# Optimization experiments

Measured on AMD Instinct MI355X. Metric: run time of the kernel, lower is better.

The kernel has to match this reference:

```python
import jax, jax.numpy as jnp
import numpy as np

D_MODEL = 1024
NUM_HEADS = 16
HEAD_DIM = D_MODEL // NUM_HEADS
B, S = 4, 2048


def setup_inputs() -> dict:
    key = jax.random.key(0)
    ks = jax.random.split(key, 11)
    scale = 1.0 / np.sqrt(D_MODEL)
    return {
        "query": jax.random.normal(ks[0], (B, S, D_MODEL), dtype=jnp.float32),
        "key": jax.random.normal(ks[1], (B, S, D_MODEL), dtype=jnp.float32),
        "value": jax.random.normal(ks[2], (B, S, D_MODEL), dtype=jnp.float32),
        "Wq": jax.random.normal(ks[3], (D_MODEL, D_MODEL), dtype=jnp.float32) * scale,
        "bq": jnp.zeros((D_MODEL,), dtype=jnp.float32),
        "Wk": jax.random.normal(ks[4], (D_MODEL, D_MODEL), dtype=jnp.float32) * scale,
        "bk": jnp.zeros((D_MODEL,), dtype=jnp.float32),
        "Wv": jax.random.normal(ks[5], (D_MODEL, D_MODEL), dtype=jnp.float32) * scale,
        "bv": jnp.zeros((D_MODEL,), dtype=jnp.float32),
        "Wo": jax.random.normal(ks[6], (D_MODEL, D_MODEL), dtype=jnp.float32) * scale,
        "bo": jnp.zeros((D_MODEL,), dtype=jnp.float32),
    }


def reference(query, key, value, Wq, bq, Wk, bk, Wv, bv, Wo, bo):
    b = query.shape[0]
    # QKV projections, split into heads: [B, H, S, hd]
    Q = (query @ Wq + bq).reshape(b, -1, NUM_HEADS, HEAD_DIM).transpose(0, 2, 1, 3)
    K = (key @ Wk + bk).reshape(b, -1, NUM_HEADS, HEAD_DIM).transpose(0, 2, 1, 3)
    V = (value @ Wv + bv).reshape(b, -1, NUM_HEADS, HEAD_DIM).transpose(0, 2, 1, 3)
    # scaled dot-product attention, full [B, H, S, S] scores (as in original)
    scores = jnp.einsum("bhqd,bhkd->bhqk", Q, K) / jnp.sqrt(
        jnp.asarray(HEAD_DIM, dtype=jnp.float32))
    attn = jax.nn.softmax(scores, axis=-1)
    out = jnp.einsum("bhqk,bhkd->bhqd", attn, V)
    out = out.transpose(0, 2, 1, 3).reshape(b, -1, D_MODEL)
    return out @ Wo + bo
```

## Files before the change

### kernel.cpp

```cpp
#include <hip/hip_runtime.h>
#include <hip/hip_bf16.h>

typedef _Float16 f16;
typedef _Float16 f16x8 __attribute__((ext_vector_type(8)));
typedef _Float16 f16x4 __attribute__((ext_vector_type(4)));
typedef __fp16 h16x2 __attribute__((ext_vector_type(2)));
typedef float f32x4 __attribute__((ext_vector_type(4)));

#define D_MODEL 1024
#define NHEAD 16
#define HD 64
#define BATCH 4
#define SEQ 2048
#define TOK (BATCH * SEQ)

__device__ __forceinline__ void gload_lds16(const void* g, void* l) {
  __builtin_amdgcn_global_load_lds(
      (const __attribute__((address_space(1))) unsigned int*)g,
      (__attribute__((address_space(3))) unsigned int*)l, 16, 0, 0);
}

__device__ __forceinline__ f16x8 fragF16_64(const char* rowptr, int g, int c) {
  union { uint4 u; f16x8 v; } r;
  r.u = *reinterpret_cast<const uint4*>(rowptr + ((g * 16) ^ ((c & 3) << 4)));
  return r.v;
}
__device__ __forceinline__ f16x8 fragF32_128(const char* rowptr, int g, int c) {
  const int s = (c & 7) << 4;
  union { uint4 u; float f[4]; } a, b;
  a.u = *reinterpret_cast<const uint4*>(rowptr + ((g * 32) ^ s));
  b.u = *reinterpret_cast<const uint4*>(rowptr + ((g * 32 + 16) ^ s));
  f16x8 r;
  r[0] = (f16)a.f[0]; r[1] = (f16)a.f[1]; r[2] = (f16)a.f[2]; r[3] = (f16)a.f[3];
  r[4] = (f16)b.f[0]; r[5] = (f16)b.f[1]; r[6] = (f16)b.f[2]; r[7] = (f16)b.f[3];
  return r;
}
__device__ __forceinline__ f16x8 lds_frag(const char* rowptr, int cb0, int s) {
  const uint2 a = *reinterpret_cast<const uint2*>(rowptr + (cb0 ^ s));
  const uint2 b = *reinterpret_cast<const uint2*>(rowptr + ((cb0 + 32) ^ s));
  union { unsigned int u[4]; f16x8 v; } r;
  r.u[0] = a.x; r.u[1] = a.y; r.u[2] = b.x; r.u[3] = b.y;
  return r.v;
}

__global__ __launch_bounds__(256) void transpose_cvt4_k(
    const float* __restrict__ w0, const float* __restrict__ w1,
    const float* __restrict__ w2, const float* __restrict__ w3,
    f16* __restrict__ t0, f16* __restrict__ t1, f16* __restrict__ t2,
    f16* __restrict__ t3) {
  __shared__ float tile[32][33];
  const float* W = blockIdx.z == 0 ? w0 : blockIdx.z == 1 ? w1 : blockIdx.z == 2 ? w2 : w3;
  f16* Wt = blockIdx.z == 0 ? t0 : blockIdx.z == 1 ? t1 : blockIdx.z == 2 ? t2 : t3;
  int n0 = blockIdx.x * 32, k0 = blockIdx.y * 32;
  int tx = threadIdx.x & 31, ty = threadIdx.x >> 5;
#pragma unroll
  for (int i = 0; i < 32; i += 8)
    tile[ty + i][tx] = W[(size_t)(k0 + ty + i) * D_MODEL + n0 + tx];
  __syncthreads();
#pragma unroll
  for (int i = 0; i < 32; i += 8)
    Wt[(size_t)(n0 + ty + i) * D_MODEL + k0 + tx] = (f16)tile[tx][ty + i];
}

template <bool A_F32, bool B_F32, bool OUT_F32, bool BIAS_ROW>
__global__ __launch_bounds__(256) void gemm_k(
    const void* __restrict__ Ap, const void* __restrict__ Bp,
    const float* __restrict__ bias, void* __restrict__ Cout,
    int M, int N, int K, float scale) {
  constexpr int ABUF = A_F32 ? 16384 : 8192;
  constexpr int BBUF = B_F32 ? 16384 : 8192;
  constexpr int BUF = ABUF + BBUF;
  constexpr int NA = A_F32 ? 4 : 2;
  constexpr int NB = B_F32 ? 4 : 2;
  __shared__ char smem[2 * BUF];
  const int tid = threadIdx.x;
  const int lane = tid & 63, wid = tid >> 6;
  const int g = lane >> 4, c = lane & 15;
  const int wm = wid >> 1, wn = wid & 1;
  const size_t brow = (size_t)blockIdx.y * 128, bcol = (size_t)blockIdx.x * 128;

  f32x4 acc[4][4];
#pragma unroll
  for (int i = 0; i < 4; ++i)
#pragma unroll
    for (int j = 0; j < 4; ++j) acc[i][j] = (f32x4){0.f, 0.f, 0.f, 0.f};

  const char* ga[NA];
  const char* gb[NB];
#pragma unroll
  for (int j = 0; j < NA; ++j) {
    int ch = wid * NA + j;
    if constexpr (A_F32) {
      int row = ch * 8 + (lane >> 3);
      ga[j] = (const char*)Ap + ((size_t)(brow + row) * K) * 4 +
              (((lane & 7) * 16) ^ ((row & 7) << 4));
    } else {
      int row = ch * 16 + (lane >> 2);
      ga[j] = (const char*)Ap + ((size_t)(brow + row) * K) * 2 +
              (((lane & 3) * 16) ^ ((row & 3) << 4));
    }
  }
#pragma unroll
  for (int j = 0; j < NB; ++j) {
    int ch = wid * NB + j;
    if constexpr (B_F32) {
      int row = ch * 8 + (lane >> 3);
      gb[j] = (const char*)Bp + ((size_t)(bcol + row) * K) * 4 +
              (((lane & 7) * 16) ^ ((row & 7) << 4));
    } else {
      int row = ch * 16 + (lane >> 2);
      gb[j] = (const char*)Bp + ((size_t)(bcol + row) * K) * 2 +
              (((lane & 3) * 16) ^ ((row & 3) << 4));
    }
  }
  auto stage = [&](char* buf) {
#pragma unroll
    for (int j = 0; j < NA; ++j) {
      gload_lds16(ga[j], buf + (wid * NA + j) * 1024);
      ga[j] += A_F32 ? 128 : 64;
    }
#pragma unroll
    for (int j = 0; j < NB; ++j) {
      gload_lds16(gb[j], buf + ABUF + (wid * NB + j) * 1024);
      gb[j] += B_F32 ? 128 : 64;
    }
  };

  stage(smem);
  const int nt = K / 32;
  for (int t = 0; t < nt; ++t) {
    char* cur = smem + (size_t)(t & 1) * BUF;
    char* nxt = smem + (size_t)((t + 1) & 1) * BUF;
    asm volatile("s_waitcnt vmcnt(0)" ::: "memory");
    __syncthreads();
    if (t + 1 < nt) stage(nxt);

    f16x8 Af[4], Bf[4];
#pragma unroll
    for (int fm = 0; fm < 4; ++fm) {
      int row = wm * 64 + fm * 16 + c;
      if constexpr (A_F32) Af[fm] = fragF32_128(cur + row * 128, g, c);
      else Af[fm] = fragF16_64(cur + row * 64, g, c);
    }
#pragma unroll
    for (int fn = 0; fn < 4; ++fn) {
      int row = wn * 64 + fn * 16 + c;
      if constexpr (B_F32) Bf[fn] = fragF32_128(cur + ABUF + row * 128, g, c);
      else Bf[fn] = fragF16_64(cur + ABUF + row * 64, g, c);
    }
#pragma unroll
    for (int fm = 0; fm < 4; ++fm)
#pragma unroll
      for (int fn = 0; fn < 4; ++fn)
        acc[fm][fn] = __builtin_amdgcn_mfma_f32_16x16x32_f16(Af[fm], Bf[fn],
                                                             acc[fm][fn], 0, 0, 0);
  }

#pragma unroll
  for (int fn = 0; fn < 4; ++fn) {
    size_t col = bcol + wn * 64 + fn * 16 + c;
    float cbias = BIAS_ROW ? 0.f : bias[col];
#pragma unroll
    for (int fm = 0; fm < 4; ++fm) {
#pragma unroll
      for (int r = 0; r < 4; ++r) {
        size_t row = brow + wm * 64 + fm * 16 + g * 4 + r;
        float v = (acc[fm][fn][r] + (BIAS_ROW ? bias[row] : cbias)) * scale;
        if (OUT_F32)
          ((float*)Cout)[row * (size_t)N + col] = v;
        else
          ((f16*)Cout)[row * (size_t)N + col] = (f16)v;
      }
    }
  }
}

__global__ __launch_bounds__(512) void attn_k(const f16* __restrict__ Q,
                                              const f16* __restrict__ Kp,
                                              const f16* __restrict__ Vt,
                                              f16* __restrict__ AO) {
  __shared__ char smem[32768];
  const int tid = threadIdx.x, lane = tid & 63, wid = tid >> 6;
  const int g = lane >> 4, c = lane & 15;
  const int b = blockIdx.x >> 4, h = blockIdx.x & 15;
  const int qt = blockIdx.y;
  const size_t qrow0 = (size_t)b * SEQ + (size_t)qt * 256;
  const int sr = lane >> 3;
  const int sc = (lane & 7) * 16;
  const float NEG_M = -8.65617025f;

#pragma unroll
  for (int j = 0; j < 4; ++j) {
    int ch = wid * 4 + j;
    int row = ch * 8 + sr;
    const char* gq = (const char*)Q + ((qrow0 + row) * D_MODEL + h * HD) * 2 +
                     (sc ^ (sr << 4));
    gload_lds16(gq, smem + ch * 1024);
  }
  asm volatile("s_waitcnt vmcnt(0)" ::: "memory");
  __syncthreads();

  f16x8 Qf[2][2];
#pragma unroll
  for (int fq = 0; fq < 2; ++fq) {
    int row = wid * 32 + fq * 16 + c;
#pragma unroll
    for (int kk = 0; kk < 2; ++kk) {
      union { uint4 u; f16x8 v; } r;
      r.u = *reinterpret_cast<const uint4*>(
          smem + row * 128 + ((kk * 64 + g * 16) ^ ((c & 7) << 4)));
      Qf[fq][kk] = r.v;
    }
  }
  __syncthreads();

  const char* gk;
  const char* gv;
  {
    int row = wid * 8 + sr;
    gk = (const char*)Kp + (((size_t)b * SEQ + row) * D_MODEL + h * HD) * 2 +
         (sc ^ (sr << 4));
    gv = (const char*)Vt + ((size_t)(h * HD + row) * TOK + (size_t)b * SEQ) * 2 +
         (sc ^ (sr << 4));
  }
  gload_lds16(gk, smem + wid * 1024);
  gload_lds16(gv, smem + 8192 + wid * 1024);
  gk += (size_t)64 * D_MODEL * 2;
  gv += 64 * 2;

  f16x8 ones_f;
#pragma unroll
  for (int j = 0; j < 8; ++j) ones_f[j] = (c == 0) ? (f16)1.0f : (f16)0.0f;

  f32x4 o[4][2];
#pragma unroll
  for (int i = 0; i < 4; ++i)
#pragma unroll
    for (int j = 0; j < 2; ++j) o[i][j] = (f32x4){0.f, 0.f, 0.f, 0.f};
  f32x4 o_l[2] = {(f32x4){0.f, 0.f, 0.f, 0.f}, (f32x4){0.f, 0.f, 0.f, 0.f}};

  for (int t = 0; t < SEQ / 64; ++t) {
    char* cur = smem + (size_t)(t & 1) * 16384;
    char* nxt = smem + (size_t)((t + 1) & 1) * 16384;
    asm volatile("s_waitcnt vmcnt(0)" ::: "memory");
    __syncthreads();
    if (t + 1 < SEQ / 64) {
      gload_lds16(gk, nxt + wid * 1024);
      gload_lds16(gv, nxt + 8192 + wid * 1024);
      gk += (size_t)64 * D_MODEL * 2;
      gv += 64 * 2;
    }
    const char* Ks = cur;
    const char* Vs = cur + 8192;

    f32x4 st[4][2];
#pragma unroll
    for (int i = 0; i < 4; ++i)
#pragma unroll
      for (int j = 0; j < 2; ++j)
        st[i][j] = (f32x4){NEG_M, NEG_M, NEG_M, NEG_M};
#pragma unroll
    for (int kk = 0; kk < 2; ++kk) {
      f16x8 Kf[4];
#pragma unroll
      for (int km = 0; km < 4; ++km) {
        int row = km * 16 + c;
        union { uint4 u; f16x8 v; } r;
        r.u = *reinterpret_cast<const uint4*>(
            Ks + row * 128 + ((kk * 64 + g * 16) ^ ((c & 7) << 4)));
        Kf[km] = r.v;
      }
      __builtin_amdgcn_s_setprio(1);
#pragma unroll
      for (int km = 0; km < 4; ++km)
#pragma unroll
        for (int fq = 0; fq < 2; ++fq)
          st[km][fq] = __builtin_amdgcn_mfma_f32_16x16x32_f16(Kf[km], Qf[fq][kk],
                                                              st[km][fq], 0, 0, 0);
      __builtin_amdgcn_s_setprio(0);
    }

    f16x8 pb[2][2];
#pragma unroll
    for (int fq = 0; fq < 2; ++fq) {
#pragma unroll
      for (int km = 0; km < 4; ++km)
#pragma unroll
        for (int r = 0; r < 4; ++r)
          st[km][fq][r] = __builtin_amdgcn_exp2f(st[km][fq][r]);
#pragma unroll
      for (int k2 = 0; k2 < 2; ++k2) {
        union { h16x2 h2[4]; f16x8 v; } u;
        u.h2[0] = __builtin_amdgcn_cvt_pkrtz(st[2 * k2][fq][0], st[2 * k2][fq][1]);
        u.h2[1] = __builtin_amdgcn_cvt_pkrtz(st[2 * k2][fq][2], st[2 * k2][fq][3]);
        u.h2[2] = __builtin_amdgcn_cvt_pkrtz(st[2 * k2 + 1][fq][0], st[2 * k2 + 1][fq][1]);
        u.h2[3] = __builtin_amdgcn_cvt_pkrtz(st[2 * k2 + 1][fq][2], st[2 * k2 + 1][fq][3]);
        pb[k2][fq] = u.v;
      }
    }

#pragma unroll
    for (int k2 = 0; k2 < 2; ++k2) {
      f16x8 Vf[4];
#pragma unroll
      for (int fhd = 0; fhd < 4; ++fhd) {
        int row = fhd * 16 + c;
        Vf[fhd] = lds_frag(Vs + row * 128, k2 * 64 + g * 8, (row & 7) << 4);
      }
      __builtin_amdgcn_s_setprio(1);
#pragma unroll
      for (int fhd = 0; fhd < 4; ++fhd)
#pragma unroll
        for (int fq = 0; fq < 2; ++fq)
          o[fhd][fq] = __builtin_amdgcn_mfma_f32_16x16x32_f16(Vf[fhd], pb[k2][fq],
                                                              o[fhd][fq], 0, 0, 0);
#pragma unroll
      for (int fq = 0; fq < 2; ++fq)
        o_l[fq] = __builtin_amdgcn_mfma_f32_16x16x32_f16(ones_f, pb[k2][fq],
                                                         o_l[fq], 0, 0, 0);
      __builtin_amdgcn_s_setprio(0);
    }
  }

#pragma unroll
  for (int fq = 0; fq < 2; ++fq) {
    float L = __shfl(o_l[fq][0], c);
    float rl = 1.0f / L;
    size_t token = qrow0 + wid * 32 + fq * 16 + c;
#pragma unroll
    for (int fhd = 0; fhd < 4; ++fhd) {
      f16x4 vv;
#pragma unroll
      for (int r = 0; r < 4; ++r) vv[r] = (f16)(o[fhd][fq][r] * rl);
      *reinterpret_cast<f16x4*>(AO + token * D_MODEL + h * HD + fhd * 16 + g * 4) = vv;
    }
  }
}

extern "C" void kernel_launch(void* const* d_in, const int* in_sizes, int n_in,
                              void* d_out, int out_size, void* d_ws, size_t ws_size,
                              hipStream_t stream) {
  const float* q32 = (const float*)d_in[0];
  const float* k32 = (const float*)d_in[1];
  const float* v32 = (const float*)d_in[2];
  const float* Wq = (const float*)d_in[3];
  const float* bq = (const float*)d_in[4];
  const float* Wk = (const float*)d_in[5];
  const float* bk = (const float*)d_in[6];
  const float* Wv = (const float*)d_in[7];
  const float* bv = (const float*)d_in[8];
  const float* Wo = (const float*)d_in[9];
  const float* bo = (const float*)d_in[10];

  const size_t TOKD = (size_t)TOK * D_MODEL;
  const size_t WD = (size_t)D_MODEL * D_MODEL;
  f16* Qp = (f16*)d_ws;
  f16* Kp = Qp + TOKD;
  f16* Vt = Kp + TOKD;
  f16* AO = Vt + TOKD;
  f16* Wqt = AO + TOKD;
  f16* Wkt = Wqt + WD;
  f16* Wvt = Wkt + WD;
  f16* Wot = Wvt + WD;

  dim3 tg(32, 32, 4);
  transpose_cvt4_k<<<tg, 256, 0, stream>>>(Wq, Wk, Wv, Wo, Wqt, Wkt, Wvt, Wot);

  dim3 gq(D_MODEL / 128, TOK / 128);
  gemm_k<true, false, false, false><<<gq, 256, 0, stream>>>(
      q32, Wqt, bq, Qp, TOK, D_MODEL, D_MODEL, 0.18033688f);
  gemm_k<true, false, false, false><<<gq, 256, 0, stream>>>(
      k32, Wkt, bk, Kp, TOK, D_MODEL, D_MODEL, 1.0f);
  dim3 gv(TOK / 128, D_MODEL / 128);
  gemm_k<false, true, false, true><<<gv, 256, 0, stream>>>(
      Wvt, v32, bv, Vt, D_MODEL, TOK, D_MODEL, 1.0f);

  dim3 ga(BATCH * NHEAD, SEQ / 256);
  attn_k<<<ga, 512, 0, stream>>>(Qp, Kp, Vt, AO);

  gemm_k<false, false, true, false><<<gq, 256, 0, stream>>>(
      AO, Wot, bo, (float*)d_out, TOK, D_MODEL, D_MODEL, 1.0f);
}
```

Before: 228.1 us.

## Deepen attention K/V prefetch to four stages and use 8-wave GEMM blocks

The attention kernel's K/V staging goes from double buffering to a 4-slot ring with three tiles in flight. Partial vmcnt waits let it consume the oldest tile while newer loads are still pending, which is meant to hide global-load latency; LDS use doubles to 64 KB per block. Separately, the GEMM kernel moves from 256 to 512 threads per 128x128 tile, with each wave computing a 32x64 sub-tile instead of 64x64. This gives more waves for latency hiding but halves MFMA work per fragment load.

```diff
diff --git a/kernel.cpp b/kernel.cpp
--- a/kernel.cpp
+++ b/kernel.cpp
@@ -63,15 +63,15 @@
 }
 
 template <bool A_F32, bool B_F32, bool OUT_F32, bool BIAS_ROW>
-__global__ __launch_bounds__(256) void gemm_k(
+__global__ __launch_bounds__(512) void gemm_k(
     const void* __restrict__ Ap, const void* __restrict__ Bp,
     const float* __restrict__ bias, void* __restrict__ Cout,
     int M, int N, int K, float scale) {
   constexpr int ABUF = A_F32 ? 16384 : 8192;
   constexpr int BBUF = B_F32 ? 16384 : 8192;
   constexpr int BUF = ABUF + BBUF;
-  constexpr int NA = A_F32 ? 4 : 2;
-  constexpr int NB = B_F32 ? 4 : 2;
+  constexpr int NA = A_F32 ? 2 : 1;
+  constexpr int NB = B_F32 ? 2 : 1;
   __shared__ char smem[2 * BUF];
   const int tid = threadIdx.x;
   const int lane = tid & 63, wid = tid >> 6;
@@ -79,9 +79,9 @@
   const int wm = wid >> 1, wn = wid & 1;
   const size_t brow = (size_t)blockIdx.y * 128, bcol = (size_t)blockIdx.x * 128;
 
-  f32x4 acc[4][4];
-#pragma unroll
-  for (int i = 0; i < 4; ++i)
+  f32x4 acc[2][4];
+#pragma unroll
+  for (int i = 0; i < 2; ++i)
 #pragma unroll
     for (int j = 0; j < 4; ++j) acc[i][j] = (f32x4){0.f, 0.f, 0.f, 0.f};
 
@@ -135,10 +135,10 @@
     __syncthreads();
     if (t + 1 < nt) stage(nxt);
 
-    f16x8 Af[4], Bf[4];
-#pragma unroll
-    for (int fm = 0; fm < 4; ++fm) {
-      int row = wm * 64 + fm * 16 + c;
+    f16x8 Af[2], Bf[4];
+#pragma unroll
+    for (int fm = 0; fm < 2; ++fm) {
+      int row = wm * 32 + fm * 16 + c;
       if constexpr (A_F32) Af[fm] = fragF32_128(cur + row * 128, g, c);
       else Af[fm] = fragF16_64(cur + row * 64, g, c);
     }
@@ -149,7 +149,7 @@
       else Bf[fn] = fragF16_64(cur + ABUF + row * 64, g, c);
     }
 #pragma unroll
-    for (int fm = 0; fm < 4; ++fm)
+    for (int fm = 0; fm < 2; ++fm)
 #pragma unroll
       for (int fn = 0; fn < 4; ++fn)
         acc[fm][fn] = __builtin_amdgcn_mfma_f32_16x16x32_f16(Af[fm], Bf[fn],
@@ -161,10 +161,10 @@
     size_t col = bcol + wn * 64 + fn * 16 + c;
     float cbias = BIAS_ROW ? 0.f : bias[col];
 #pragma unroll
-    for (int fm = 0; fm < 4; ++fm) {
+    for (int fm = 0; fm < 2; ++fm) {
 #pragma unroll
       for (int r = 0; r < 4; ++r) {
-        size_t row = brow + wm * 64 + fm * 16 + g * 4 + r;
+        size_t row = brow + wm * 32 + fm * 16 + g * 4 + r;
         float v = (acc[fm][fn][r] + (BIAS_ROW ? bias[row] : cbias)) * scale;
         if (OUT_F32)
           ((float*)Cout)[row * (size_t)N + col] = v;
@@ -179,7 +179,7 @@
                                               const f16* __restrict__ Kp,
                                               const f16* __restrict__ Vt,
                                               f16* __restrict__ AO) {
-  __shared__ char smem[32768];
+  __shared__ char smem[65536];
   const int tid = threadIdx.x, lane = tid & 63, wid = tid >> 6;
   const int g = lane >> 4, c = lane & 15;
   const int b = blockIdx.x >> 4, h = blockIdx.x & 15;
@@ -188,6 +188,7 @@
   const int sr = lane >> 3;
   const int sc = (lane & 7) * 16;
   const float NEG_M = -8.65617025f;
+  constexpr int NT = SEQ / 64;
 
 #pragma unroll
   for (int j = 0; j < 4; ++j) {
@@ -223,10 +224,13 @@
     gv = (const char*)Vt + ((size_t)(h * HD + row) * TOK + (size_t)b * SEQ) * 2 +
          (sc ^ (sr << 4));
   }
-  gload_lds16(gk, smem + wid * 1024);
-  gload_lds16(gv, smem + 8192 + wid * 1024);
-  gk += (size_t)64 * D_MODEL * 2;
-  gv += 64 * 2;
+#pragma unroll
+  for (int tt = 0; tt < 3; ++tt) {
+    gload_lds16(gk, smem + tt * 8192 + wid * 1024);
+    gload_lds16(gv, smem + 32768 + tt * 8192 + wid * 1024);
+    gk += (size_t)64 * D_MODEL * 2;
+    gv += 64 * 2;
+  }
 
   f16x8 ones_f;
 #pragma unroll
@@ -239,19 +243,23 @@
     for (int j = 0; j < 2; ++j) o[i][j] = (f32x4){0.f, 0.f, 0.f, 0.f};
   f32x4 o_l[2] = {(f32x4){0.f, 0.f, 0.f, 0.f}, (f32x4){0.f, 0.f, 0.f, 0.f}};
 
-  for (int t = 0; t < SEQ / 64; ++t) {
-    char* cur = smem + (size_t)(t & 1) * 16384;
-    char* nxt = smem + (size_t)((t + 1) & 1) * 16384;
-    asm volatile("s_waitcnt vmcnt(0)" ::: "memory");
-    __syncthreads();
-    if (t + 1 < SEQ / 64) {
-      gload_lds16(gk, nxt + wid * 1024);
-      gload_lds16(gv, nxt + 8192 + wid * 1024);
+  for (int t = 0; t < NT; ++t) {
+    if (t < NT - 2)
+      asm volatile("s_waitcnt vmcnt(4)" ::: "memory");
+    else if (t == NT - 2)
+      asm volatile("s_waitcnt vmcnt(2)" ::: "memory");
+    else
+      asm volatile("s_waitcnt vmcnt(0)" ::: "memory");
+    __builtin_amdgcn_s_barrier();
+    asm volatile("" ::: "memory");
+    if (t + 3 < NT) {
+      gload_lds16(gk, smem + ((t + 3) & 3) * 8192 + wid * 1024);
+      gload_lds16(gv, smem + 32768 + ((t + 3) & 3) * 8192 + wid * 1024);
       gk += (size_t)64 * D_MODEL * 2;
       gv += 64 * 2;
     }
-    const char* Ks = cur;
-    const char* Vs = cur + 8192;
+    const char* Ks = smem + (t & 3) * 8192;
+    const char* Vs = smem + 32768 + (t & 3) * 8192;
 
     f32x4 st[4][2];
 #pragma unroll
@@ -367,17 +375,17 @@
   transpose_cvt4_k<<<tg, 256, 0, stream>>>(Wq, Wk, Wv, Wo, Wqt, Wkt, Wvt, Wot);
 
   dim3 gq(D_MODEL / 128, TOK / 128);
-  gemm_k<true, false, false, false><<<gq, 256, 0, stream>>>(
+  gemm_k<true, false, false, false><<<gq, 512, 0, stream>>>(
       q32, Wqt, bq, Qp, TOK, D_MODEL, D_MODEL, 0.18033688f);
-  gemm_k<true, false, false, false><<<gq, 256, 0, stream>>>(
+  gemm_k<true, false, false, false><<<gq, 512, 0, stream>>>(
       k32, Wkt, bk, Kp, TOK, D_MODEL, D_MODEL, 1.0f);
   dim3 gv(TOK / 128, D_MODEL / 128);
-  gemm_k<false, true, false, true><<<gv, 256, 0, stream>>>(
+  gemm_k<false, true, false, true><<<gv, 512, 0, stream>>>(
       Wvt, v32, bv, Vt, D_MODEL, TOK, D_MODEL, 1.0f);
 
   dim3 ga(BATCH * NHEAD, SEQ / 256);
   attn_k<<<ga, 512, 0, stream>>>(Qp, Kp, Vt, AO);
 
-  gemm_k<false, false, true, false><<<gq, 256, 0, stream>>>(
+  gemm_k<false, false, true, false><<<gq, 512, 0, stream>>>(
       AO, Wot, bo, (float*)d_out, TOK, D_MODEL, D_MODEL, 1.0f);
 }
```

After: 230.5 us. Within noise of the previous version (+1.1%).
